# Kernel tuning notes

Hardware: AMD Instinct MI355X
Metric: run time of the kernel (lower is better)

Reference implementation:

```python
import jax, jax.numpy as jnp
import numpy as np

B, C, T = 16, 129, 2000
NF, ED, K = 40, 64, 16

def setup_inputs() -> dict:
    key = jax.random.key(0)
    ks = iter(jax.random.split(key, 48))
    def n(shape, s=0.05):
        return jax.random.normal(next(ks), shape, jnp.float32) * s
    inp = {
        'x': jax.random.normal(next(ks), (B, C, T), jnp.float32),
        # temporal conv (1,25) pad (0,12) + BN (inference running stats)
        'tconv_w': n((NF, 1, 1, 25)), 'tconv_b': jnp.zeros((NF,)),
        'tbn_g': jnp.ones((NF,)), 'tbn_b': jnp.zeros((NF,)), 'tbn_m': n((NF,)), 'tbn_v': jnp.ones((NF,)),
        # spatial conv (C,1) + BN
        'sconv_w': n((NF, NF, C, 1)), 'sconv_b': jnp.zeros((NF,)),
        'sbn_g': jnp.ones((NF,)), 'sbn_b': jnp.zeros((NF,)), 'sbn_m': n((NF,)), 'sbn_v': jnp.ones((NF,)),
        # separable: depthwise (1,15) pad (0,7), pointwise 1x1 -> 2*NF, BN
        'dw_w': n((NF, 1, 1, 15)), 'dw_b': jnp.zeros((NF,)),
        'pw_w': n((2 * NF, NF, 1, 1)), 'pw_b': jnp.zeros((2 * NF,)),
        'pbn_g': jnp.ones((2 * NF,)), 'pbn_b': jnp.zeros((2 * NF,)), 'pbn_m': n((2 * NF,)), 'pbn_v': jnp.ones((2 * NF,)),
        # projection 2*NF -> ED
        'proj_w': n((ED, 2 * NF)), 'proj_b': jnp.zeros((ED,)),
        # ENN cell 0 (input ED)
        'wx0': n((K, ED)), 'L0': jnp.eye(K, dtype=jnp.float32) + 0.1 * n((K, K), 1.0),
        'll0': jnp.asarray(np.log(0.1), jnp.float32), 'b0': jnp.zeros((K,)),
        'ln0_g': jnp.ones((K,)), 'ln0_b': jnp.zeros((K,)),
        # ENN cell 1 (input K)
        'wx1': n((K, K)), 'L1': jnp.eye(K, dtype=jnp.float32) + 0.1 * n((K, K), 1.0),
        'll1': jnp.asarray(np.log(0.1), jnp.float32), 'b1': jnp.zeros((K,)),
        'ln1_g': jnp.ones((K,)), 'ln1_b': jnp.zeros((K,)),
        # collapse
        'wq_w': n((K, K)), 'wq_b': jnp.zeros((K,)), 'log_temp': jnp.asarray(0.0, jnp.float32),
    }
    return inp

def _conv(x, w, b, pad, groups=1):
    y = jax.lax.conv_general_dilated(
        x, w, window_strides=(1, 1), padding=pad,
        dimension_numbers=('NCHW', 'OIHW', 'NCHW'), feature_group_count=groups)
    return y + b[None, :, None, None]

def _bn(x, g, b, m, v, eps=1e-5):
    inv = g / jnp.sqrt(v + eps)
    return x * inv[None, :, None, None] + (b - m * inv)[None, :, None, None]

def _cell(x, h, Wx, L, ll, b, g, be, eps=1e-5):
    E = L @ L.T  # PSD entanglement matrix [K,K]
    pre = x @ Wx.T + h @ E.T - jnp.exp(ll) * h + b
    mu = pre.mean(-1, keepdims=True)
    var = pre.var(-1, keepdims=True)
    pre = (pre - mu) / jnp.sqrt(var + eps) * g + be
    return jnp.tanh(pre)

def _forward(x, tconv_w, tconv_b, tbn_g, tbn_b, tbn_m, tbn_v,
             sconv_w, sconv_b, sbn_g, sbn_b, sbn_m, sbn_v,
             dw_w, dw_b, pw_w, pw_b, pbn_g, pbn_b, pbn_m, pbn_v,
             proj_w, proj_b,
             wx0, L0, ll0, b0, ln0_g, ln0_b,
             wx1, L1, ll1, b1, ln1_g, ln1_b,
             wq_w, wq_b, log_temp):
    # ---- SpatialCNN front-end (BN in inference mode, dropout=identity) ----
    o = x[:, None, :, :]                                        # [B,1,C,T]
    o = _conv(o, tconv_w, tconv_b, ((0, 0), (12, 12)))          # [B,NF,C,T]
    o = jax.nn.elu(_bn(o, tbn_g, tbn_b, tbn_m, tbn_v))
    o = _conv(o, sconv_w, sconv_b, ((0, 0), (0, 0)))            # [B,NF,1,T]
    o = jax.nn.elu(_bn(o, sbn_g, sbn_b, sbn_m, sbn_v))
    o = _conv(o, dw_w, dw_b, ((0, 0), (7, 7)), groups=NF)       # depthwise
    o = _conv(o, pw_w, pw_b, ((0, 0), (0, 0)))                  # [B,2NF,1,T]
    o = jax.nn.elu(_bn(o, pbn_g, pbn_b, pbn_m, pbn_v))
    Bn, Ch, _, Tt = o.shape
    o = o.reshape(Bn, Ch, Tt // 4, 4).mean(-1)                  # AvgPool (1,4) -> [B,2NF,T']
    feats = o.transpose(0, 2, 1) @ proj_w.T + proj_b            # [B,T',ED]
    # ---- Entangled RNN over T' steps (lax.scan) ----
    h_init = (jnp.zeros((Bn, K), feats.dtype), jnp.zeros((Bn, K), feats.dtype))
    def step(carry, xt):
        h0, h1 = carry
        h0 = _cell(xt, h0, wx0, L0, ll0, b0, ln0_g, ln0_b)
        h1 = _cell(h0, h1, wx1, L1, ll1, b1, ln1_g, ln1_b)
        return (h0, h1), None
    (h0, h1), _ = jax.lax.scan(step, h_init, feats.transpose(1, 0, 2))
    Z = h1                                                       # [B,K]
    # ---- Collapse attention ----
    q = Z @ wq_w.T + wq_b
    scores = jnp.sum(q * Z, axis=-1, keepdims=True)              # [B,1]
    alpha = jax.nn.softmax(scores / jnp.exp(log_temp), axis=-1)  # [B,1]
    return Z, alpha

def reference(x, tconv_w, tconv_b, tbn_g, tbn_b, tbn_m, tbn_v,
              sconv_w, sconv_b, sbn_g, sbn_b, sbn_m, sbn_v,
              dw_w, dw_b, pw_w, pw_b, pbn_g, pbn_b, pbn_m, pbn_v,
              proj_w, proj_b,
              wx0, L0, ll0, b0, ln0_g, ln0_b,
              wx1, L1, ll1, b1, ln1_g, ln1_b,
              wq_w, wq_b, log_temp):
    return _forward(x, tconv_w, tconv_b, tbn_g, tbn_b, tbn_m, tbn_v,
                    sconv_w, sconv_b, sbn_g, sbn_b, sbn_m, sbn_v,
                    dw_w, dw_b, pw_w, pw_b, pbn_g, pbn_b, pbn_m, pbn_v,
                    proj_w, proj_b,
                    wx0, L0, ll0, b0, ln0_g, ln0_b,
                    wx1, L1, ll1, b1, ln1_g, ln1_b,
                    wq_w, wq_b, log_temp)
```

## Files before the change

kernel.cpp:

```cpp
#include <hip/hip_runtime.h>
#include <math.h>

#define B_ 16
#define C_ 129
#define T_ 2000
#define NF_ 40
#define ED_ 64
#define K_ 16
#define TP_ 500

#define OFF_SB2 1040
#define OFF_PWC 1088
#define OFF_PB2 4288
#define OFF_WP  4368
#define OFF_BP  5648
#define OFF_M0  5664
#define OFF_M1  5920
#define OFF_W1A 6224
#define OFF_W2U 8192
#define OFF_XP  1495040
#define OFF_S2R 1623040

typedef __attribute__((ext_vector_type(8))) short s8v;
typedef __attribute__((ext_vector_type(4))) float f4v;

#define XROW 292

__device__ __forceinline__ float elu_f(float x) {
    return x > 0.f ? x : (__expf(x) - 1.f);
}
__device__ __forceinline__ float tanh2_f(float a2) {
    return fmaf(-2.f, __builtin_amdgcn_rcpf(__expf(a2) + 1.f), 1.f);
}
__device__ __forceinline__ unsigned bfr(float v) {
    return (__float_as_uint(v) + 0x8000u) >> 16;
}

#define DPPF(v, ctrl) __int_as_float(__builtin_amdgcn_update_dpp( \
    0, __float_as_int(v), (ctrl), 0xF, 0xF, false))
#define DPPI(v, ctrl) __builtin_amdgcn_update_dpp(0, (v), (ctrl), 0xF, 0xF, false)

#define RSUM16(s) do {                     \
    s += DPPF(s, 0x128);                   \
    s += DPPF(s, 0x124);                   \
    s += DPPF(s, 0x122);                   \
    s += DPPF(s, 0x121);                   \
} while (0)

struct P0 {
    const float *tconv_w, *tconv_b, *tbn_g, *tbn_b, *tbn_m, *tbn_v;
    const float *sconv_b, *sbn_g, *sbn_b, *sbn_m, *sbn_v;
    const float *pw_w, *pw_b, *pbn_g, *pbn_b, *pbn_m, *pbn_v;
    const float *proj_w, *proj_b, *wx0, *b0, *L0, *ll0, *L1, *ll1;
    const float *sconv_w;
    float* ws;
};

__global__ __launch_bounds__(256) void k0_all(P0 p) {
    const int tid = threadIdx.x;
    float* ws = p.ws;
    const float eps = 1e-5f;

    if (blockIdx.x < 1250) {
        const int i = blockIdx.x * 256 + tid;
        if (i < 320000)
            ((float4*)(ws + OFF_S2R))[i] = make_float4(0.f, 0.f, 0.f, 0.f);
        return;
    }
    if (blockIdx.x < 1444) {
        const int e = (blockIdx.x - 1250) * 256 + tid;
        if (e >= C_ * 3 * 2 * 64) return;
        unsigned short* w2b = (unsigned short*)(ws + OFF_W2U);
        const int c = e / 384;
        int r = e - c * 384;
        const int mt = r >> 7; r &= 127;
        const int kc = r >> 6;
        const int lane = r & 63;
        const int g = mt * 16 + (lane & 15);
        const float sinv = (g < NF_) ? p.sbn_g[g] * rsqrtf(p.sbn_v[g] + 1e-5f) : 0.f;
        unsigned short o[8];
#pragma unroll
        for (int j = 0; j < 8; ++j) {
            const int f = kc * 32 + (lane >> 4) * 8 + j;
            float v = 0.f;
            if (g < NF_ && f < NF_) v = p.sconv_w[g * (NF_ * C_) + f * C_ + c] * sinv;
            o[j] = (unsigned short)bfr(v);
        }
        unsigned short* dst = w2b + (size_t)e * 8;
#pragma unroll
        for (int j = 0; j < 8; ++j) dst[j] = o[j];
        return;
    }

    const int gtid = (blockIdx.x - 1444) * 256 + tid;
    const int stride = 8 * 256;
    for (int e = gtid; e < 192; e += stride) {
        const int mt = e >> 6, L = e & 63;
        const int f = mt * 16 + (L & 15);
        float inv = 0.f, bias = 0.f;
        if (f < NF_) {
            inv = p.tbn_g[f] / sqrtf(p.tbn_v[f] + eps);
            bias = p.tconv_b[f] * inv + p.tbn_b[f] - p.tbn_m[f] * inv;
        }
        unsigned short* dst = ((unsigned short*)(ws + OFF_W1A)) + e * 8;
#pragma unroll
        for (int j = 0; j < 8; ++j) {
            const int k = (L >> 4) * 8 + j;
            float v = 0.f;
            if (f < NF_) {
                if (k < 25) v = p.tconv_w[f * 25 + k] * inv;
                else if (k == 25) v = bias;
            }
            dst[j] = (unsigned short)bfr(v);
        }
    }
    for (int f = gtid; f < NF_; f += stride) {
        const float sinv = p.sbn_g[f] / sqrtf(p.sbn_v[f] + eps);
        ws[OFF_SB2 + f] = p.sconv_b[f] * sinv + p.sbn_b[f] - p.sbn_m[f] * sinv;
    }
    for (int e = gtid; e < 3200; e += stride) {
        const int g = e / 40;
        const float pinv = p.pbn_g[g] / sqrtf(p.pbn_v[g] + eps);
        ws[OFF_PWC + e] = p.pw_w[e] * pinv;
    }
    for (int g = gtid; g < 80; g += stride) {
        const float pinv = p.pbn_g[g] / sqrtf(p.pbn_v[g] + eps);
        ws[OFF_PB2 + g] = p.pw_b[g] * pinv + p.pbn_b[g] - p.pbn_m[g] * pinv;
    }
    for (int e = gtid; e < 1280; e += stride) {
        const int k = e / 80, g = e - k * 80;
        float a = 0.f;
        for (int ee = 0; ee < ED_; ++ee)
            a = fmaf(p.wx0[k * ED_ + ee], p.proj_w[ee * 80 + g], a);
        ws[OFF_WP + e] = a;
    }
    for (int k = gtid; k < K_; k += stride) {
        float a = p.b0[k];
        for (int ee = 0; ee < ED_; ++ee)
            a = fmaf(p.wx0[k * ED_ + ee], p.proj_b[ee], a);
        ws[OFF_BP + k] = a;
    }
    for (int e = gtid; e < 256; e += stride) {
        const int k = e >> 4, j = e & 15;
        float a0 = 0.f, a1 = 0.f;
        for (int i = 0; i < 16; ++i) {
            a0 = fmaf(p.L0[k * 16 + i], p.L0[j * 16 + i], a0);
            a1 = fmaf(p.L1[k * 16 + i], p.L1[j * 16 + i], a1);
        }
        if (k == j) { a0 -= expf(p.ll0[0]); a1 -= expf(p.ll1[0]); }
        ws[OFF_M0 + e] = a0;
        ws[OFF_M1 + e] = a1;
    }
}

__global__ __launch_bounds__(256, 4) void k1_mfma(
    const float* __restrict__ x, const unsigned short* __restrict__ w1a,
    const unsigned short* __restrict__ w2b, float* __restrict__ s2raw) {
    __shared__ float xs[17 * XROW];
    __shared__ unsigned int vsI[2048];

    const int tid = threadIdx.x;
    const int split = blockIdx.x & 7;
    const int tile = (blockIdx.x >> 3) & 7;
    const int b = blockIdx.x >> 6;
    const int c0 = (split * C_) >> 3;
    const int c1 = ((split + 1) * C_) >> 3;
    const int cc = c1 - c0;
    const int t0 = tile << 8;
    const int w = tid >> 6;
    const int lane = tid & 63;
    const int n = lane & 15;
    const int q = lane >> 4;
    const int qh = q >> 1;
    const int q1_2 = (q & 1) * 2;
    const bool q3 = (q == 3);
    const int wb = w << 9;
    const int w64 = w << 6;
    const int ln8 = n + q * 8;

    for (int i = tid; i < 2048; i += 256) vsI[i] = 0u;
    for (int e = tid; e < cc * XROW; e += 256) {
        const int cl = e / XROW;
        const int i = e - cl * XROW;
        const int t = t0 - 12 + i;
        float v = 0.f;
        if ((unsigned)t < (unsigned)T_) v = x[(b * C_ + c0 + cl) * T_ + t];
        xs[e] = v;
    }
    __syncthreads();

    const s8v* w1a8 = (const s8v*)w1a;
    s8v wA[3];
#pragma unroll
    for (int mt = 0; mt < 3; ++mt) wA[mt] = w1a8[mt * 64 + lane];

    f4v acc[4][3];
#pragma unroll
    for (int nt = 0; nt < 4; ++nt)
#pragma unroll
        for (int mt = 0; mt < 3; ++mt) acc[nt][mt] = (f4v)0.f;

    const s8v* w2b8 = (const s8v*)w2b;
    const f4v z4 = (f4v)0.f;

    for (int cl = 0; cl < cc; ++cl) {
        const int c = c0 + cl;
        s8v af[3][2];
#pragma unroll
        for (int mt = 0; mt < 3; ++mt)
#pragma unroll
            for (int kc = 0; kc < 2; ++kc)
                af[mt][kc] = w2b8[((c * 3 + mt) * 2 + kc) * 64 + lane];

        const float* xrow = &xs[cl * XROW + w64 + ln8];

#pragma unroll
        for (int nt = 0; nt < 4; ++nt) {
            float bx[8];
#pragma unroll
            for (int j = 0; j < 8; ++j) bx[j] = xrow[nt * 16 + j];
            if (q3) bx[1] = 1.0f;
            unsigned pw_[4];
#pragma unroll
            for (int jj = 0; jj < 4; ++jj)
                pw_[jj] = bfr(bx[2 * jj]) |
                    ((__float_as_uint(bx[2 * jj + 1]) + 0x8000u) & 0xFFFF0000u);
            const s8v bh = *(const s8v*)pw_;
#pragma unroll
            for (int mt = 0; mt < 3; ++mt) {
                const f4v vT = __builtin_amdgcn_mfma_f32_16x16x32_bf16(
                    wA[mt], bh, z4, 0, 0, 0);
                const float e0 = elu_f(vT[0]);
                const float e1 = elu_f(vT[1]);
                const float e2 = elu_f(vT[2]);
                const float e3 = elu_f(vT[3]);
                const unsigned lo = bfr(e0) |
                    ((__float_as_uint(e1) + 0x8000u) & 0xFFFF0000u);
                const unsigned hi = bfr(e2) |
                    ((__float_as_uint(e3) + 0x8000u) & 0xFFFF0000u);
                const int base = wb + ((2 * mt + qh) << 6) + (n << 2) + q1_2;
                vsI[base] = lo;
                vsI[base + 1] = hi;
            }
            __builtin_amdgcn_wave_barrier();
            const s8v b0 = *(const s8v*)&vsI[wb + (q << 6) + (n << 2)];
            const s8v b1 = *(const s8v*)&vsI[wb + ((4 + q) << 6) + (n << 2)];
#pragma unroll
            for (int mt = 0; mt < 3; ++mt) {
                acc[nt][mt] = __builtin_amdgcn_mfma_f32_16x16x32_bf16(
                    af[mt][0], b0, acc[nt][mt], 0, 0, 0);
                acc[nt][mt] = __builtin_amdgcn_mfma_f32_16x16x32_bf16(
                    af[mt][1], b1, acc[nt][mt], 0, 0, 0);
            }
            __builtin_amdgcn_wave_barrier();
        }
    }

#pragma unroll
    for (int nt = 0; nt < 4; ++nt) {
        const int t = t0 + w * 64 + nt * 16 + n;
        if (t >= T_) continue;
#pragma unroll
        for (int mt = 0; mt < 3; ++mt) {
#pragma unroll
            for (int r = 0; r < 4; ++r) {
                const int g = mt * 16 + q * 4 + r;
                if (g < NF_)
                    atomicAdd(&s2raw[(b * NF_ + g) * T_ + t], acc[nt][mt][r]);
            }
        }
    }
}

__global__ __launch_bounds__(256) void k2_dwpw(
    const float* __restrict__ s2raw, const float* __restrict__ sb2,
    const float* __restrict__ dw_w, const float* __restrict__ dw_b,
    const float* __restrict__ pwc, const float* __restrict__ pb2,
    const float* __restrict__ WP, const float* __restrict__ bp,
    float* __restrict__ xp) {
    __shared__ float st[NF_ * 114];
    __shared__ float dwo[NF_ * 100];
    __shared__ float dwwl[NF_ * 15];
    __shared__ float dwbl[NF_];
    __shared__ float pwcl[80 * 40];
    __shared__ float pb2l[80];
    __shared__ float WPl[K_ * 80];
    __shared__ float bpl[K_];
    __shared__ float po[80 * 25];
    const int tid = threadIdx.x;
    const int b = blockIdx.x / 20;
    const int tp0 = (blockIdx.x % 20) * 25;
    const int tbase = tp0 * 4 - 7;
    for (int e = tid; e < NF_ * 114; e += 256) {
        const int f = e / 114;
        const int i = e - f * 114;
        const int t = tbase + i;
        float v = 0.f;
        if ((unsigned)t < (unsigned)T_)
            v = elu_f(s2raw[(b * NF_ + f) * T_ + t] + sb2[f]);
        st[e] = v;
    }
    for (int e = tid; e < 600; e += 256) dwwl[e] = dw_w[e];
    for (int e = tid; e < 3200; e += 256) pwcl[e] = pwc[e];
    for (int e = tid; e < 1280; e += 256) WPl[e] = WP[e];
    if (tid < NF_) dwbl[tid] = dw_b[tid];
    if (tid < 80) pb2l[tid] = pb2[tid];
    if (tid < K_) bpl[tid] = bp[tid];
    __syncthreads();
    for (int e = tid; e < 4000; e += 256) {
        const int f = e / 100;
        const int tq = e - f * 100;
        float a = dwbl[f];
#pragma unroll
        for (int kk = 0; kk < 15; ++kk)
            a = fmaf(dwwl[f * 15 + kk], st[f * 114 + tq + kk], a);
        dwo[e] = a;
    }
    __syncthreads();
    for (int e = tid; e < 2000; e += 256) {
        const int g = e / 25;
        const int tp = e - g * 25;
        float sum = 0.f;
#pragma unroll
        for (int dt = 0; dt < 4; ++dt) {
            float a = pb2l[g];
            for (int f = 0; f < NF_; ++f)
                a = fmaf(pwcl[g * 40 + f], dwo[f * 100 + tp * 4 + dt], a);
            sum += elu_f(a);
        }
        po[e] = sum * 0.25f;
    }
    __syncthreads();
    for (int e = tid; e < 400; e += 256) {
        const int tp = e >> 4;
        const int k = e & 15;
        float a = bpl[k];
        for (int g = 0; g < 80; ++g)
            a = fmaf(WPl[k * 80 + g], po[g * 25 + tp], a);
        xp[(b * TP_ + tp0 + tp) * K_ + k] = a;
    }
}

#define SCAN_STEP(I, S) do {                                              \
    float vB = h0cur;                                                     \
    float a0 = 0.f, a1 = 0.f, c0 = 0.f, c1 = 0.f;                         \
    _Pragma("unroll")                                                     \
    for (int j = 0; j < 16; j += 2) {                                     \
        vA = DPPF(vA, 0x121);  a0 = fmaf(W1[j], vA, a0);                  \
        vB = DPPF(vB, 0x121);  c0 = fmaf(W2[j], vB, c0);                  \
        vA = DPPF(vA, 0x121);  a1 = fmaf(W1[j + 1], vA, a1);              \
        vB = DPPF(vB, 0x121);  c1 = fmaf(W2[j + 1], vB, c1);              \
    }                                                                     \
    const float xv = xn[S];                                               \
    int tf = (I) + 5; if (tf > TP_ - 1) tf = TP_ - 1;                     \
    xn[S] = xpb[tf * K_];                                                 \
    const float cadd = lower ? b1r : xv;                                  \
    const float pre = ((a0 + a1) + (c0 + c1)) + cadd;                     \
    float s1 = pre, s2 = pre * pre;                                       \
    RSUM16(s1);                                                           \
    RSUM16(s2);                                                           \
    const float mu = s1 * 0.0625f;                                        \
    const float var = fmaf(s2, 0.0625f, -mu * mu);                        \
    float hn = tanh2_f(fmaf((pre - mu) * rsqrtf(var + 1e-5f), gg, bb));   \
    if ((I) == 0 && lower) hn = 0.f;                                      \
    vA = hn;                                                              \
    h0cur = h0pend;                                                       \
    h0pend = __shfl(hn, 32 + k, 64);                                      \
    if ((I) == 500) h1out = vA;                                           \
} while (0)

__global__ __launch_bounds__(64, 1) void k3_scan(
    const float* __restrict__ xp, const float* __restrict__ M0,
    const float* __restrict__ M1, const float* __restrict__ wx1,
    const float* __restrict__ b1, const float* __restrict__ ln0_g,
    const float* __restrict__ ln0_b, const float* __restrict__ ln1_g,
    const float* __restrict__ ln1_b, float* __restrict__ out) {
    const int lane = threadIdx.x;
    const int k = lane & 15;
    const bool lower = lane < 32;
    const int b = blockIdx.x;

    float W1[16], W2[16];
    {
        int pid = k;
#pragma unroll
        for (int j = 0; j < 16; ++j) {
            pid = DPPI(pid, 0x121);
            const float m0 = M0[k * 16 + pid];
            const float m1 = M1[k * 16 + pid];
            const float wx = wx1[k * 16 + pid];
            W1[j] = lower ? m1 : m0;
            W2[j] = lower ? wx : 0.f;
        }
    }
    const float b1r = b1[k];
    const float g0 = 2.f * ln0_g[k], be0 = 2.f * ln0_b[k];
    const float gg = lower ? 2.f * ln1_g[k] : g0;
    const float bb = lower ? 2.f * ln1_b[k] : be0;
    const float* xpb = xp + b * TP_ * K_ + k;

    float h0_0;
    {
        const float x0 = xpb[0];
        float s1 = x0, s2 = x0 * x0;
        RSUM16(s1);
        RSUM16(s2);
        const float mu = s1 * 0.0625f;
        const float var = fmaf(s2, 0.0625f, -mu * mu);
        h0_0 = tanh2_f(fmaf((x0 - mu) * rsqrtf(var + 1e-5f), g0, be0));
    }
    float vA = lower ? 0.f : h0_0;
    float h0cur = 0.f;
    float h0pend = h0_0;
    float h1out = 0.f;

    float xn[4];
    xn[0] = xpb[1 * K_];
    xn[1] = xpb[2 * K_];
    xn[2] = xpb[3 * K_];
    xn[3] = xpb[4 * K_];

    for (int i = 0; i < 504; i += 4) {
        SCAN_STEP(i + 0, 0);
        SCAN_STEP(i + 1, 1);
        SCAN_STEP(i + 2, 2);
        SCAN_STEP(i + 3, 3);
    }
    if (lane < 16) {
        out[b * K_ + k] = h1out;
        if (k == 0) out[256 + b] = 1.0f;
    }
}

extern "C" void kernel_launch(void* const* d_in, const int* in_sizes, int n_in,
                              void* d_out, int out_size, void* d_ws, size_t ws_size,
                              hipStream_t stream) {
    const float* x       = (const float*)d_in[0];
    const float* dw_w    = (const float*)d_in[13];
    const float* dw_b    = (const float*)d_in[14];
    const float* wx1     = (const float*)d_in[29];
    const float* b1      = (const float*)d_in[32];
    const float* ln0_g   = (const float*)d_in[27];
    const float* ln0_b   = (const float*)d_in[28];
    const float* ln1_g   = (const float*)d_in[33];
    const float* ln1_b   = (const float*)d_in[34];
    float* ws = (float*)d_ws;
    float* out = (float*)d_out;

    P0 p;
    p.tconv_w = (const float*)d_in[1]; p.tconv_b = (const float*)d_in[2];
    p.tbn_g = (const float*)d_in[3]; p.tbn_b = (const float*)d_in[4];
    p.tbn_m = (const float*)d_in[5]; p.tbn_v = (const float*)d_in[6];
    p.sconv_b = (const float*)d_in[8];
    p.sbn_g = (const float*)d_in[9]; p.sbn_b = (const float*)d_in[10];
    p.sbn_m = (const float*)d_in[11]; p.sbn_v = (const float*)d_in[12];
    p.pw_w = (const float*)d_in[15]; p.pw_b = (const float*)d_in[16];
    p.pbn_g = (const float*)d_in[17]; p.pbn_b = (const float*)d_in[18];
    p.pbn_m = (const float*)d_in[19]; p.pbn_v = (const float*)d_in[20];
    p.proj_w = (const float*)d_in[21]; p.proj_b = (const float*)d_in[22];
    p.wx0 = (const float*)d_in[23]; p.b0 = (const float*)d_in[26];
    p.L0 = (const float*)d_in[24]; p.ll0 = (const float*)d_in[25];
    p.L1 = (const float*)d_in[30]; p.ll1 = (const float*)d_in[31];
    p.sconv_w = (const float*)d_in[7];
    p.ws = ws;

    unsigned short* w2b = (unsigned short*)(ws + OFF_W2U);
    unsigned short* w1a = (unsigned short*)(ws + OFF_W1A);

    k0_all<<<dim3(1452), dim3(256), 0, stream>>>(p);
    k1_mfma<<<dim3(1024), dim3(256), 0, stream>>>(x, w1a, w2b, ws + OFF_S2R);
    k2_dwpw<<<dim3(320), dim3(256), 0, stream>>>(ws + OFF_S2R, ws + OFF_SB2,
                                                 dw_w, dw_b, ws + OFF_PWC,
                                                 ws + OFF_PB2, ws + OFF_WP, ws + OFF_BP,
                                                 ws + OFF_XP);
    k3_scan<<<dim3(16), dim3(64), 0, stream>>>(ws + OFF_XP, ws + OFF_M0, ws + OFF_M1,
                                               wx1, b1, ln0_g, ln0_b, ln1_g, ln1_b, out);
}
```

Before: 368.7 us.

## Broadcast recurrent hidden state via readlane instead of DPP rotation and shuffle

The serial ENN scan now broadcasts the previous hidden states of both cells into scalar registers with readlane, then does plain FMAs against unrotated weight rows. This replaces the DPP-rotated matvec and the per-step cross-lane shuffle that staged the cell-0 state for the lower lanes. The lower cell now reads the cell-0 state straight from the previous step's register. The loop drops from 504 to 500 iterations. The intent is to shorten the per-step latency chain of the recurrence, at the cost of 32 readlane instructions per step and their SGPR-to-VALU hazard waits.

```diff
diff --git a/kernel.cpp b/kernel.cpp
--- a/kernel.cpp
+++ b/kernel.cpp
@@ -38,7 +38,6 @@
 
 #define DPPF(v, ctrl) __int_as_float(__builtin_amdgcn_update_dpp( \
     0, __float_as_int(v), (ctrl), 0xF, 0xF, false))
-#define DPPI(v, ctrl) __builtin_amdgcn_update_dpp(0, (v), (ctrl), 0xF, 0xF, false)
 
 #define RSUM16(s) do {                     \
     s += DPPF(s, 0x128);                   \
@@ -46,6 +45,8 @@
     s += DPPF(s, 0x122);                   \
     s += DPPF(s, 0x121);                   \
 } while (0)
+
+#define RDLANE(v, L) __int_as_float(__builtin_amdgcn_readlane(__float_as_int(v), (L)))
 
 struct P0 {
     const float *tconv_w, *tconv_b, *tbn_g, *tbn_b, *tbn_m, *tbn_v;
@@ -342,14 +343,19 @@
 }
 
 #define SCAN_STEP(I, S) do {                                              \
-    float vB = h0cur;                                                     \
+    float sH0[16], sH1[16];                                               \
+    _Pragma("unroll")                                                     \
+    for (int j = 0; j < 16; ++j) {                                        \
+        sH0[j] = RDLANE(vA, 32 + j);                                      \
+        sH1[j] = RDLANE(vA, j);                                           \
+    }                                                                     \
     float a0 = 0.f, a1 = 0.f, c0 = 0.f, c1 = 0.f;                         \
     _Pragma("unroll")                                                     \
     for (int j = 0; j < 16; j += 2) {                                     \
-        vA = DPPF(vA, 0x121);  a0 = fmaf(W1[j], vA, a0);                  \
-        vB = DPPF(vB, 0x121);  c0 = fmaf(W2[j], vB, c0);                  \
-        vA = DPPF(vA, 0x121);  a1 = fmaf(W1[j + 1], vA, a1);              \
-        vB = DPPF(vB, 0x121);  c1 = fmaf(W2[j + 1], vB, c1);              \
+        a0 = fmaf(WA[j],     sH0[j],     a0);                             \
+        a1 = fmaf(WA[j + 1], sH0[j + 1], a1);                             \
+        c0 = fmaf(WB[j],     sH1[j],     c0);                             \
+        c1 = fmaf(WB[j + 1], sH1[j + 1], c1);                             \
     }                                                                     \
     const float xv = xn[S];                                               \
     int tf = (I) + 5; if (tf > TP_ - 1) tf = TP_ - 1;                     \
@@ -361,12 +367,7 @@
     RSUM16(s2);                                                           \
     const float mu = s1 * 0.0625f;                                        \
     const float var = fmaf(s2, 0.0625f, -mu * mu);                        \
-    float hn = tanh2_f(fmaf((pre - mu) * rsqrtf(var + 1e-5f), gg, bb));   \
-    if ((I) == 0 && lower) hn = 0.f;                                      \
-    vA = hn;                                                              \
-    h0cur = h0pend;                                                       \
-    h0pend = __shfl(hn, 32 + k, 64);                                      \
-    if ((I) == 500) h1out = vA;                                           \
+    vA = tanh2_f(fmaf((pre - mu) * rsqrtf(var + 1e-5f), gg, bb));         \
 } while (0)
 
 __global__ __launch_bounds__(64, 1) void k3_scan(
@@ -380,18 +381,14 @@
     const bool lower = lane < 32;
     const int b = blockIdx.x;
 
-    float W1[16], W2[16];
-    {
-        int pid = k;
-#pragma unroll
-        for (int j = 0; j < 16; ++j) {
-            pid = DPPI(pid, 0x121);
-            const float m0 = M0[k * 16 + pid];
-            const float m1 = M1[k * 16 + pid];
-            const float wx = wx1[k * 16 + pid];
-            W1[j] = lower ? m1 : m0;
-            W2[j] = lower ? wx : 0.f;
-        }
+    float WA[16], WB[16];
+#pragma unroll
+    for (int j = 0; j < 16; ++j) {
+        const float m0 = M0[k * 16 + j];
+        const float m1 = M1[k * 16 + j];
+        const float wx = wx1[k * 16 + j];
+        WA[j] = lower ? wx : m0;
+        WB[j] = lower ? m1 : 0.f;
     }
     const float b1r = b1[k];
     const float g0 = 2.f * ln0_g[k], be0 = 2.f * ln0_b[k];
@@ -410,9 +407,6 @@
         h0_0 = tanh2_f(fmaf((x0 - mu) * rsqrtf(var + 1e-5f), g0, be0));
     }
     float vA = lower ? 0.f : h0_0;
-    float h0cur = 0.f;
-    float h0pend = h0_0;
-    float h1out = 0.f;
 
     float xn[4];
     xn[0] = xpb[1 * K_];
@@ -420,14 +414,14 @@
     xn[2] = xpb[3 * K_];
     xn[3] = xpb[4 * K_];
 
-    for (int i = 0; i < 504; i += 4) {
+    for (int i = 0; i < TP_; i += 4) {
         SCAN_STEP(i + 0, 0);
         SCAN_STEP(i + 1, 1);
         SCAN_STEP(i + 2, 2);
         SCAN_STEP(i + 3, 3);
     }
     if (lane < 16) {
-        out[b * K_ + k] = h1out;
+        out[b * K_ + k] = vA;
         if (k == 0) out[256 + b] = 1.0f;
     }
 }
```

After: 363.4 us. Within noise of the previous version (-1.4%).
